# Kernel optimization log

Hardware: AMD Instinct MI355X
Metric: run time of the kernel (lower is better)

The kernel has to match this reference:

```python
import jax, jax.numpy as jnp
import numpy as np

B, C, H, W = 8, 256, 64, 64
CI = 128  # inter_channels = in_channels // reduction

def _conv1x1(x, w, b):
    # x: [b, c, h, w], w: [o, c], b: [o]
    return jnp.einsum('bchw,oc->bohw', x, w) + b[None, :, None, None]

def setup_inputs() -> dict:
    key = jax.random.key(0)
    ks = jax.random.split(key, 5)
    s_in = 1.0 / np.sqrt(C)
    s_ci = 1.0 / np.sqrt(CI)
    return {
        'x': jax.random.normal(ks[0], (B, C, H, W), jnp.float32),
        'w_g': jax.random.normal(ks[1], (CI, C), jnp.float32) * s_in,
        'b_g': jnp.zeros((CI,), jnp.float32),
        'w_theta': jax.random.normal(ks[2], (CI, C), jnp.float32) * s_in,
        'b_theta': jnp.zeros((CI,), jnp.float32),
        'w_phi': jax.random.normal(ks[3], (CI, C), jnp.float32) * s_in,
        'b_phi': jnp.zeros((CI,), jnp.float32),
        'w_out': jax.random.normal(ks[4], (C, CI), jnp.float32) * s_ci,
        'b_out': jnp.zeros((C,), jnp.float32),
    }

def reference(x, w_g, b_g, w_theta, b_theta, w_phi, b_phi, w_out, b_out):
    n, c, h, w = x.shape
    N = h * w
    g_x = _conv1x1(x, w_g, b_g).reshape(n, CI, N).transpose(0, 2, 1)        # [b, N, ci]
    theta_x = _conv1x1(x, w_theta, b_theta).reshape(n, CI, N).transpose(0, 2, 1)  # [b, N, ci]
    phi_x = _conv1x1(x, w_phi, b_phi).reshape(n, CI, N)                     # [b, ci, N]
    pw = jnp.einsum('bnc,bcm->bnm', theta_x, phi_x)                         # [b, N, N]
    # Faithful to source: divides by ci**(-0.5) == multiplies by sqrt(ci)
    pw = pw / (jnp.asarray(CI, x.dtype) ** -0.5)
    pw = jax.nn.softmax(pw, axis=-1)
    y = jnp.einsum('bnm,bmc->bnc', pw, g_x)                                 # [b, N, ci]
    y = y.transpose(0, 2, 1).reshape(n, CI, h, w)
    return x + _conv1x1(y, w_out, b_out)
```

## Files before the change

kernel.cpp:

```cpp
#include <hip/hip_runtime.h>
#include <hip/hip_bf16.h>
#include <stdint.h>
#include <stddef.h>


typedef __bf16 bf16;
typedef __attribute__((ext_vector_type(8))) __bf16 bf16x8;
typedef __attribute__((ext_vector_type(4))) __bf16 bf16x4;
typedef __attribute__((ext_vector_type(4))) float  f32x4;
typedef __attribute__((ext_vector_type(4))) int    i32x4;

#define MFMA16(a, b, c) __builtin_amdgcn_mfma_f32_16x16x32_bf16((a), (b), (c), 0, 0, 0)

constexpr int NB  = 8;
constexpr int NC  = 256;
constexpr int NN  = 4096;
constexpr int NCI = 128;
constexpr size_t NEL = (size_t)NB * NN * NCI;

__global__ __launch_bounds__(256) void k_proj(
    const float* __restrict__ x,
    const float* __restrict__ wt, const float* __restrict__ bt,
    const float* __restrict__ wp, const float* __restrict__ bp,
    const float* __restrict__ wg, const float* __restrict__ bg,
    bf16* __restrict__ qh, bf16* __restrict__ ql,
    bf16* __restrict__ kh, bf16* __restrict__ kl,
    bf16* __restrict__ vv)
{
    const int nt  = blockIdx.x;
    const int pj  = blockIdx.y;
    const int b   = blockIdx.z;
    const int tid = threadIdx.x;
    const int wv  = tid >> 6;
    const int ln  = tid & 63;
    const int lg  = ln >> 4;
    const int lq  = ln & 15;

    const float* W;
    const float* bias;
    if (pj == 0)      { W = wt; bias = bt; }
    else if (pj == 1) { W = wp; bias = bp; }
    else              { W = wg; bias = bg; }
    const bool split = (pj != 2);

    __shared__ char lds[49152];
    char* Ah = lds;
    char* Al = lds + 8192;
    char* Wh = lds + 16384;
    char* Wl = lds + 32768;

    f32x4 acc[8];
#pragma unroll
    for (int j = 0; j < 8; ++j) acc[j] = f32x4{0.f, 0.f, 0.f, 0.f};

    const int n0 = nt * 64;

    for (int c0 = 0; c0 < NC; c0 += 64) {
        __syncthreads();
#pragma unroll
        for (int p = 0; p < 4; ++p) {
            int cc = p * 16 + (tid >> 4);
            int nn = (tid & 15) * 4;
            f32x4 xv = *(const f32x4*)(x + ((size_t)b * NC + (c0 + cc)) * NN + n0 + nn);
#pragma unroll
            for (int e = 0; e < 4; ++e) {
                float f = xv[e];
                bf16 h = (bf16)f;
                int row = nn + e;
                int off = (row * 128 + cc * 2) ^ ((row & 7) << 4);
                *(bf16*)(Ah + off) = h;
                *(bf16*)(Al + off) = (bf16)(f - (float)h);
            }
        }
#pragma unroll
        for (int p = 0; p < 8; ++p) {
            int i  = p * 16 + (tid >> 4);
            int c4 = (tid & 15) * 4;
            f32x4 w4 = *(const f32x4*)(W + (size_t)i * NC + c0 + c4);
            bf16x4 hv, lv;
#pragma unroll
            for (int e = 0; e < 4; ++e) {
                bf16 h = (bf16)w4[e];
                hv[e] = h;
                lv[e] = (bf16)(w4[e] - (float)h);
            }
            int off = (i * 128 + c4 * 2) ^ ((i & 7) << 4);
            *(bf16x4*)(Wh + off) = hv;
            if (split) *(bf16x4*)(Wl + off) = lv;
        }
        __syncthreads();
#pragma unroll
        for (int kk = 0; kk < 2; ++kk) {
            int row  = wv * 16 + lq;
            int koff = kk * 64 + lg * 16;
            int aoff = (row * 128 + koff) ^ ((row & 7) << 4);
            bf16x8 ah = *(const bf16x8*)(Ah + aoff);
            bf16x8 al = *(const bf16x8*)(Al + aoff);
#pragma unroll
            for (int j = 0; j < 8; ++j) {
                int ir   = j * 16 + lq;
                int woff = (ir * 128 + koff) ^ ((ir & 7) << 4);
                bf16x8 bh = *(const bf16x8*)(Wh + woff);
                acc[j] = MFMA16(ah, bh, acc[j]);
                if (split) {
                    bf16x8 bl = *(const bf16x8*)(Wl + woff);
                    acc[j] = MFMA16(ah, bl, acc[j]);
                    acc[j] = MFMA16(al, bh, acc[j]);
                }
            }
        }
    }

    if (pj == 2) {
        __syncthreads();
        char* T = lds;
#pragma unroll
        for (int j = 0; j < 8; ++j) {
            int i = j * 16 + lq;
            float bv = bias[i];
#pragma unroll
            for (int r = 0; r < 4; ++r) {
                int nl = wv * 16 + lg * 4 + r;
                int off = (i * 128 + nl * 2) ^ ((i & 7) << 4);
                *(bf16*)(T + off) = (bf16)(acc[j][r] + bv);
            }
        }
        __syncthreads();
#pragma unroll
        for (int p = 0; p < 4; ++p) {
            int i  = p * 32 + (tid >> 3);
            int sl = tid & 7;
            i32x4 t = *(const i32x4*)(T + ((i * 128 + sl * 16) ^ ((i & 7) << 4)));
            *(i32x4*)(vv + ((size_t)b * NCI + i) * NN + n0 + sl * 8) = t;
        }
    } else {
#pragma unroll
        for (int j = 0; j < 8; ++j) {
            int i = j * 16 + lq;
            float bv = bias[i];
#pragma unroll
            for (int r = 0; r < 4; ++r) {
                int q = n0 + wv * 16 + lg * 4 + r;
                size_t off = ((size_t)b * NN + q) * NCI + i;
                float val = acc[j][r] + bv;
                bf16 h = (bf16)val;
                bf16 l = (bf16)(val - (float)h);
                if (pj == 0) { qh[off] = h; ql[off] = l; }
                else         { kh[off] = h; kl[off] = l; }
            }
        }
    }
}

__global__ __launch_bounds__(256, 2) void k_attn(
    const bf16* __restrict__ qh, const bf16* __restrict__ ql,
    const bf16* __restrict__ kh, const bf16* __restrict__ kl,
    const bf16* __restrict__ vt, bf16* __restrict__ y)
{
    const int bid = blockIdx.x;
    const int b   = bid & 7;
    const int qt  = bid >> 3;
    const int tid = threadIdx.x;
    const int wv  = tid >> 6;
    const int ln  = tid & 63;
    const int lg  = ln >> 4;
    const int lq  = ln & 15;
    const int n0  = qt * 64;

    __shared__ char lds[57344];
    char* KH = lds;
    char* KL = lds + 16384;
    char* VT = lds + 32768;
    char* P  = lds + 49152 + wv * 2048;

    bf16x8 qhf[4], qlf[4];
    {
        int qrow = n0 + wv * 16 + lq;
        const bf16* bh = qh + ((size_t)b * NN + qrow) * NCI;
        const bf16* bl = ql + ((size_t)b * NN + qrow) * NCI;
#pragma unroll
        for (int kk = 0; kk < 4; ++kk) {
            int d0 = kk * 32 + lg * 8;
            qhf[kk] = *(const bf16x8*)(bh + d0);
            qlf[kk] = *(const bf16x8*)(bl + d0);
        }
    }

    f32x4 o[8];
#pragma unroll
    for (int j = 0; j < 8; ++j) o[j] = f32x4{0.f, 0.f, 0.f, 0.f};
    float mrun = -1e30f, lrun = 0.f;
    const float scale = 11.313708498984761f;

    for (int m0 = 0; m0 < NN; m0 += 64) {
        __syncthreads();
#pragma unroll
        for (int p = 0; p < 4; ++p) {
            int mm = p * 16 + (tid >> 4);
            int sl = tid & 15;
            size_t g = ((size_t)b * NN + m0 + mm) * NCI + sl * 8;
            int off = (mm * 256 + sl * 16) ^ ((mm & 7) << 4);
            *(i32x4*)(KH + off) = *(const i32x4*)(kh + g);
            *(i32x4*)(KL + off) = *(const i32x4*)(kl + g);
        }
#pragma unroll
        for (int p = 0; p < 4; ++p) {
            int d  = p * 32 + (tid >> 3);
            int sl = tid & 7;
            size_t g = ((size_t)b * NCI + d) * NN + m0 + sl * 8;
            int off = (d * 128 + sl * 16) ^ ((d & 7) << 4);
            *(i32x4*)(VT + off) = *(const i32x4*)(vt + g);
        }
        __syncthreads();

        float pv[4][4];
        __builtin_amdgcn_s_setprio(1);
#pragma unroll
        for (int jm = 0; jm < 4; ++jm) {
            f32x4 s = f32x4{0.f, 0.f, 0.f, 0.f};
            int mrow = jm * 16 + lq;
#pragma unroll
            for (int kk = 0; kk < 4; ++kk) {
                int aoff = (mrow * 256 + kk * 64 + lg * 16) ^ ((mrow & 7) << 4);
                bf16x8 ah = *(const bf16x8*)(KH + aoff);
                bf16x8 al = *(const bf16x8*)(KL + aoff);
                s = MFMA16(ah, qhf[kk], s);
                s = MFMA16(al, qhf[kk], s);
                s = MFMA16(ah, qlf[kk], s);
            }
#pragma unroll
            for (int r = 0; r < 4; ++r) pv[jm][r] = s[r] * scale;
        }
        __builtin_amdgcn_s_setprio(0);

        float tmax = pv[0][0];
#pragma unroll
        for (int jm = 0; jm < 4; ++jm)
#pragma unroll
            for (int r = 0; r < 4; ++r) tmax = fmaxf(tmax, pv[jm][r]);
        tmax = fmaxf(tmax, __shfl_xor(tmax, 16));
        tmax = fmaxf(tmax, __shfl_xor(tmax, 32));
        float mnew = fmaxf(mrun, tmax);
        float alpha = __expf(mrun - mnew);
        mrun = mnew;
        float psum = 0.f;
#pragma unroll
        for (int jm = 0; jm < 4; ++jm)
#pragma unroll
            for (int r = 0; r < 4; ++r) {
                pv[jm][r] = __expf(pv[jm][r] - mnew);
                psum += pv[jm][r];
            }
        psum += __shfl_xor(psum, 16);
        psum += __shfl_xor(psum, 32);
        lrun = lrun * alpha + psum;

#pragma unroll
        for (int jm = 0; jm < 4; ++jm) {
            bf16x4 pk;
#pragma unroll
            for (int r = 0; r < 4; ++r) pk[r] = (bf16)pv[jm][r];
            int off = (lq * 128 + (jm * 16 + lg * 4) * 2) ^ ((lq & 7) << 4);
            *(bf16x4*)(P + off) = pk;
        }

        float av[4];
#pragma unroll
        for (int r = 0; r < 4; ++r) av[r] = __shfl(alpha, lg * 4 + r);
#pragma unroll
        for (int j = 0; j < 8; ++j)
#pragma unroll
            for (int r = 0; r < 4; ++r) o[j][r] *= av[r];

        bf16x8 pa[2];
#pragma unroll
        for (int t = 0; t < 2; ++t)
            pa[t] = *(const bf16x8*)(P + ((lq * 128 + t * 64 + lg * 16) ^ ((lq & 7) << 4)));
        __builtin_amdgcn_s_setprio(1);
#pragma unroll
        for (int j = 0; j < 8; ++j) {
            int d = j * 16 + lq;
#pragma unroll
            for (int t = 0; t < 2; ++t) {
                bf16x8 bv = *(const bf16x8*)(VT + ((d * 128 + t * 64 + lg * 16) ^ ((d & 7) << 4)));
                o[j] = MFMA16(pa[t], bv, o[j]);
            }
        }
        __builtin_amdgcn_s_setprio(0);
    }

    float lr[4];
#pragma unroll
    for (int r = 0; r < 4; ++r) lr[r] = __shfl(lrun, lg * 4 + r);
#pragma unroll
    for (int j = 0; j < 8; ++j) {
        int d = j * 16 + lq;
#pragma unroll
        for (int r = 0; r < 4; ++r) {
            int q = n0 + wv * 16 + lg * 4 + r;
            y[((size_t)b * NN + q) * NCI + d] = (bf16)(o[j][r] / lr[r]);
        }
    }
}

__global__ __launch_bounds__(256) void k_out(
    const bf16* __restrict__ y, const float* __restrict__ x,
    const float* __restrict__ w_out, const float* __restrict__ b_out,
    float* __restrict__ out)
{
    const int nt  = blockIdx.x;
    const int b   = blockIdx.y;
    const int tid = threadIdx.x;
    const int wv  = tid >> 6;
    const int ln  = tid & 63;
    const int lg  = ln >> 4;
    const int lq  = ln & 15;
    const int n0  = nt * 64;

    __shared__ char Y[16384];
#pragma unroll
    for (int p = 0; p < 4; ++p) {
        int nn = p * 16 + (tid >> 4);
        int d0 = (tid & 15) * 8;
        i32x4 t = *(const i32x4*)(y + ((size_t)b * NN + n0 + nn) * NCI + d0);
        *(i32x4*)(Y + ((nn * 256 + d0 * 2) ^ ((nn & 7) << 4))) = t;
    }
    __syncthreads();

    bf16x8 af[4];
    {
        int row = wv * 16 + lq;
#pragma unroll
        for (int kk = 0; kk < 4; ++kk) {
            int koff = kk * 64 + lg * 16;
            af[kk] = *(const bf16x8*)(Y + ((row * 256 + koff) ^ ((row & 7) << 4)));
        }
    }

    f32x4 acc[16];
#pragma unroll
    for (int j = 0; j < 16; ++j) acc[j] = f32x4{0.f, 0.f, 0.f, 0.f};

#pragma unroll
    for (int j = 0; j < 16; ++j) {
        int c = j * 16 + lq;
#pragma unroll
        for (int kk = 0; kk < 4; ++kk) {
            int i0 = kk * 32 + lg * 8;
            f32x4 wa = *(const f32x4*)(w_out + (size_t)c * NCI + i0);
            f32x4 wb = *(const f32x4*)(w_out + (size_t)c * NCI + i0 + 4);
            bf16x8 bw;
#pragma unroll
            for (int e = 0; e < 4; ++e) { bw[e] = (bf16)wa[e]; bw[e + 4] = (bf16)wb[e]; }
            acc[j] = MFMA16(af[kk], bw, acc[j]);
        }
    }

#pragma unroll
    for (int j = 0; j < 16; ++j) {
        int c = j * 16 + lq;
        int nb = n0 + wv * 16 + lg * 4;
        size_t off = ((size_t)b * NC + c) * (size_t)NN + nb;
        f32x4 xv = *(const f32x4*)(x + off);
        float bo = b_out[c];
        f32x4 r;
#pragma unroll
        for (int t = 0; t < 4; ++t) r[t] = acc[j][t] + xv[t] + bo;
        *(f32x4*)(out + off) = r;
    }
}

extern "C" void kernel_launch(void* const* d_in, const int* in_sizes, int n_in,
                              void* d_out, int out_size, void* d_ws, size_t ws_size,
                              hipStream_t stream)
{
    (void)in_sizes; (void)n_in; (void)out_size; (void)ws_size;
    const float* x  = (const float*)d_in[0];
    const float* wg = (const float*)d_in[1];
    const float* bg = (const float*)d_in[2];
    const float* wt = (const float*)d_in[3];
    const float* bt = (const float*)d_in[4];
    const float* wp = (const float*)d_in[5];
    const float* bp = (const float*)d_in[6];
    const float* wo = (const float*)d_in[7];
    const float* bo = (const float*)d_in[8];
    float* out = (float*)d_out;

    char* ws = (char*)d_ws;
    bf16* qh = (bf16*)(ws);
    bf16* ql = (bf16*)(ws + NEL * 2);
    bf16* kh = (bf16*)(ws + NEL * 4);
    bf16* kl = (bf16*)(ws + NEL * 6);
    bf16* vv = (bf16*)(ws + NEL * 8);
    bf16* y  = qh;

    k_proj<<<dim3(64, 3, 8), 256, 0, stream>>>(x, wt, bt, wp, bp, wg, bg,
                                               qh, ql, kh, kl, vv);
    k_attn<<<dim3(512), 256, 0, stream>>>(qh, ql, kh, kl, vv, y);
    k_out<<<dim3(64, 8), 256, 0, stream>>>(y, x, wo, bo, out);
}
```

Baseline: 255.4 us.

## Double-buffer K/V tiles and process two query tiles per wave in attention

The attention kernel now handles 128 query rows per block, with each wave covering 32 rows, so every K/V fragment read from LDS feeds two MFMA chains. K/V tiles are double-buffered in LDS and the next tile's global loads are issued through registers while the current tile computes, which cuts the loop to one barrier per tile. Together these aim to halve LDS and global traffic per query and hide load latency. In exchange the grid drops to 256 blocks, occupancy falls to one block per CU under larger LDS and register use, and there are fewer waves to hide latency.

Measured after the change: 278.6 us. 1.09x slower.

```diff
diff --git a/kernel.cpp b/kernel.cpp
--- a/kernel.cpp
+++ b/kernel.cpp
@@ -152,7 +152,7 @@
     }
 }
 
-__global__ __launch_bounds__(256, 2) void k_attn(
+__global__ __launch_bounds__(256, 1) void k_attn(
     const bf16* __restrict__ qh, const bf16* __restrict__ ql,
     const bf16* __restrict__ kh, const bf16* __restrict__ kl,
     const bf16* __restrict__ vt, bf16* __restrict__ y)
@@ -165,140 +165,226 @@
     const int ln  = tid & 63;
     const int lg  = ln >> 4;
     const int lq  = ln & 15;
-    const int n0  = qt * 64;
-
-    __shared__ char lds[57344];
-    char* KH = lds;
-    char* KL = lds + 16384;
-    char* VT = lds + 32768;
-    char* P  = lds + 49152 + wv * 2048;
-
-    bf16x8 qhf[4], qlf[4];
-    {
-        int qrow = n0 + wv * 16 + lq;
+    const int n0  = qt * 128;
+
+    __shared__ __attribute__((aligned(16))) char lds[114688];
+    char* P = lds + 98304 + wv * 4096;
+
+    const int smm = tid >> 4;
+    const int ssl = tid & 15;
+    const int svd = tid >> 3;
+    const int svl = tid & 7;
+
+    bf16x8 qhf[2][4], qlf[2][4];
+#pragma unroll
+    for (int q2 = 0; q2 < 2; ++q2) {
+        int qrow = n0 + wv * 32 + q2 * 16 + lq;
         const bf16* bh = qh + ((size_t)b * NN + qrow) * NCI;
         const bf16* bl = ql + ((size_t)b * NN + qrow) * NCI;
 #pragma unroll
         for (int kk = 0; kk < 4; ++kk) {
-            int d0 = kk * 32 + lg * 8;
-            qhf[kk] = *(const bf16x8*)(bh + d0);
-            qlf[kk] = *(const bf16x8*)(bl + d0);
-        }
-    }
-
-    f32x4 o[8];
-#pragma unroll
-    for (int j = 0; j < 8; ++j) o[j] = f32x4{0.f, 0.f, 0.f, 0.f};
-    float mrun = -1e30f, lrun = 0.f;
+            qhf[q2][kk] = *(const bf16x8*)(bh + kk * 32 + lg * 8);
+            qlf[q2][kk] = *(const bf16x8*)(bl + kk * 32 + lg * 8);
+        }
+    }
+
+    f32x4 o[2][8];
+#pragma unroll
+    for (int q2 = 0; q2 < 2; ++q2)
+#pragma unroll
+        for (int j = 0; j < 8; ++j) o[q2][j] = f32x4{0.f, 0.f, 0.f, 0.f};
+    float mrun[2] = {-1e30f, -1e30f};
+    float lrun[2] = {0.f, 0.f};
     const float scale = 11.313708498984761f;
 
-    for (int m0 = 0; m0 < NN; m0 += 64) {
-        __syncthreads();
+    {
 #pragma unroll
         for (int p = 0; p < 4; ++p) {
-            int mm = p * 16 + (tid >> 4);
-            int sl = tid & 15;
-            size_t g = ((size_t)b * NN + m0 + mm) * NCI + sl * 8;
-            int off = (mm * 256 + sl * 16) ^ ((mm & 7) << 4);
-            *(i32x4*)(KH + off) = *(const i32x4*)(kh + g);
-            *(i32x4*)(KL + off) = *(const i32x4*)(kl + g);
+            int mm = p * 16 + smm;
+            size_t g = ((size_t)b * NN + mm) * NCI + ssl * 8;
+            i32x4 h = *(const i32x4*)(kh + g);
+            i32x4 l = *(const i32x4*)(kl + g);
+            int off = (mm * 256 + ssl * 16) ^ ((mm & 7) << 4);
+            *(i32x4*)(lds + off) = h;
+            *(i32x4*)(lds + 16384 + off) = l;
         }
 #pragma unroll
         for (int p = 0; p < 4; ++p) {
-            int d  = p * 32 + (tid >> 3);
-            int sl = tid & 7;
-            size_t g = ((size_t)b * NCI + d) * NN + m0 + sl * 8;
-            int off = (d * 128 + sl * 16) ^ ((d & 7) << 4);
-            *(i32x4*)(VT + off) = *(const i32x4*)(vt + g);
-        }
-        __syncthreads();
-
-        float pv[4][4];
+            int d = p * 32 + svd;
+            size_t g = ((size_t)b * NCI + d) * NN + svl * 8;
+            i32x4 v = *(const i32x4*)(vt + g);
+            int off = (d * 128 + svl * 16) ^ ((d & 7) << 4);
+            *(i32x4*)(lds + 32768 + off) = v;
+        }
+    }
+    __syncthreads();
+
+    for (int t = 0; t < 64; ++t) {
+        const int cur = t & 1;
+        char* KH  = lds + cur * 49152;
+        char* KL  = KH + 16384;
+        char* VT  = KH + 32768;
+        char* KHn = lds + (cur ^ 1) * 49152;
+        char* KLn = KHn + 16384;
+        char* VTn = KHn + 32768;
+        const int m0n = (t + 1) * 64;
+        const bool pre = (t < 63);
+
+        i32x4 rkh[4], rkl[4];
+        if (pre) {
+#pragma unroll
+            for (int p = 0; p < 4; ++p) {
+                size_t g = ((size_t)b * NN + m0n + p * 16 + smm) * NCI + ssl * 8;
+                rkh[p] = *(const i32x4*)(kh + g);
+                rkl[p] = *(const i32x4*)(kl + g);
+            }
+        }
+
+        f32x4 s[4][2];
         __builtin_amdgcn_s_setprio(1);
 #pragma unroll
         for (int jm = 0; jm < 4; ++jm) {
-            f32x4 s = f32x4{0.f, 0.f, 0.f, 0.f};
-            int mrow = jm * 16 + lq;
+            s[jm][0] = f32x4{0.f, 0.f, 0.f, 0.f};
+            s[jm][1] = f32x4{0.f, 0.f, 0.f, 0.f};
+            const int mrow = jm * 16 + lq;
+            const int sw = (mrow & 7) << 4;
 #pragma unroll
             for (int kk = 0; kk < 4; ++kk) {
-                int aoff = (mrow * 256 + kk * 64 + lg * 16) ^ ((mrow & 7) << 4);
+                int aoff = (mrow * 256 + kk * 64 + lg * 16) ^ sw;
                 bf16x8 ah = *(const bf16x8*)(KH + aoff);
                 bf16x8 al = *(const bf16x8*)(KL + aoff);
-                s = MFMA16(ah, qhf[kk], s);
-                s = MFMA16(al, qhf[kk], s);
-                s = MFMA16(ah, qlf[kk], s);
-            }
-#pragma unroll
-            for (int r = 0; r < 4; ++r) pv[jm][r] = s[r] * scale;
+                s[jm][0] = MFMA16(ah, qhf[0][kk], s[jm][0]);
+                s[jm][1] = MFMA16(ah, qhf[1][kk], s[jm][1]);
+                s[jm][0] = MFMA16(al, qhf[0][kk], s[jm][0]);
+                s[jm][1] = MFMA16(al, qhf[1][kk], s[jm][1]);
+                s[jm][0] = MFMA16(ah, qlf[0][kk], s[jm][0]);
+                s[jm][1] = MFMA16(ah, qlf[1][kk], s[jm][1]);
+            }
         }
         __builtin_amdgcn_s_setprio(0);
 
-        float tmax = pv[0][0];
+        i32x4 rv[4];
+        if (pre) {
+#pragma unroll
+            for (int p = 0; p < 4; ++p) {
+                int mm = p * 16 + smm;
+                int off = (mm * 256 + ssl * 16) ^ ((mm & 7) << 4);
+                *(i32x4*)(KHn + off) = rkh[p];
+                *(i32x4*)(KLn + off) = rkl[p];
+            }
+#pragma unroll
+            for (int p = 0; p < 4; ++p) {
+                size_t g = ((size_t)b * NCI + p * 32 + svd) * NN + m0n + svl * 8;
+                rv[p] = *(const i32x4*)(vt + g);
+            }
+        }
+
+        float tm[2];
+        tm[0] = s[0][0][0];
+        tm[1] = s[0][1][0];
 #pragma unroll
         for (int jm = 0; jm < 4; ++jm)
 #pragma unroll
-            for (int r = 0; r < 4; ++r) tmax = fmaxf(tmax, pv[jm][r]);
-        tmax = fmaxf(tmax, __shfl_xor(tmax, 16));
-        tmax = fmaxf(tmax, __shfl_xor(tmax, 32));
-        float mnew = fmaxf(mrun, tmax);
-        float alpha = __expf(mrun - mnew);
-        mrun = mnew;
-        float psum = 0.f;
+            for (int r = 0; r < 4; ++r) {
+                tm[0] = fmaxf(tm[0], s[jm][0][r]);
+                tm[1] = fmaxf(tm[1], s[jm][1][r]);
+            }
+#pragma unroll
+        for (int q2 = 0; q2 < 2; ++q2) {
+            tm[q2] = fmaxf(tm[q2], __shfl_xor(tm[q2], 16));
+            tm[q2] = fmaxf(tm[q2], __shfl_xor(tm[q2], 32));
+        }
+        float alpha[2], psum[2];
+#pragma unroll
+        for (int q2 = 0; q2 < 2; ++q2) {
+            float mnew = fmaxf(mrun[q2], tm[q2] * scale);
+            alpha[q2] = __expf(mrun[q2] - mnew);
+            mrun[q2] = mnew;
+            psum[q2] = 0.f;
+        }
 #pragma unroll
         for (int jm = 0; jm < 4; ++jm)
 #pragma unroll
+            for (int q2 = 0; q2 < 2; ++q2) {
+                bf16x4 pk;
+#pragma unroll
+                for (int r = 0; r < 4; ++r) {
+                    float e = __expf(s[jm][q2][r] * scale - mrun[q2]);
+                    psum[q2] += e;
+                    pk[r] = (bf16)e;
+                }
+                int row = q2 * 16 + lq;
+                int off = (row * 128 + (jm * 16 + lg * 4) * 2) ^ ((lq & 7) << 4);
+                *(bf16x4*)(P + off) = pk;
+            }
+#pragma unroll
+        for (int q2 = 0; q2 < 2; ++q2) {
+            psum[q2] += __shfl_xor(psum[q2], 16);
+            psum[q2] += __shfl_xor(psum[q2], 32);
+            lrun[q2] = lrun[q2] * alpha[q2] + psum[q2];
+        }
+
+        float av0[4], av1[4];
+#pragma unroll
+        for (int r = 0; r < 4; ++r) {
+            av0[r] = __shfl(alpha[0], lg * 4 + r);
+            av1[r] = __shfl(alpha[1], lg * 4 + r);
+        }
+#pragma unroll
+        for (int j = 0; j < 8; ++j)
+#pragma unroll
             for (int r = 0; r < 4; ++r) {
-                pv[jm][r] = __expf(pv[jm][r] - mnew);
-                psum += pv[jm][r];
-            }
-        psum += __shfl_xor(psum, 16);
-        psum += __shfl_xor(psum, 32);
-        lrun = lrun * alpha + psum;
-
-#pragma unroll
-        for (int jm = 0; jm < 4; ++jm) {
-            bf16x4 pk;
-#pragma unroll
-            for (int r = 0; r < 4; ++r) pk[r] = (bf16)pv[jm][r];
-            int off = (lq * 128 + (jm * 16 + lg * 4) * 2) ^ ((lq & 7) << 4);
-            *(bf16x4*)(P + off) = pk;
-        }
-
-        float av[4];
-#pragma unroll
-        for (int r = 0; r < 4; ++r) av[r] = __shfl(alpha, lg * 4 + r);
-#pragma unroll
-        for (int j = 0; j < 8; ++j)
-#pragma unroll
-            for (int r = 0; r < 4; ++r) o[j][r] *= av[r];
-
-        bf16x8 pa[2];
-#pragma unroll
-        for (int t = 0; t < 2; ++t)
-            pa[t] = *(const bf16x8*)(P + ((lq * 128 + t * 64 + lg * 16) ^ ((lq & 7) << 4)));
+                o[0][j][r] *= av0[r];
+                o[1][j][r] *= av1[r];
+            }
+
+        bf16x8 pa[2][2];
+#pragma unroll
+        for (int q2 = 0; q2 < 2; ++q2)
+#pragma unroll
+            for (int tt = 0; tt < 2; ++tt) {
+                int row = q2 * 16 + lq;
+                pa[q2][tt] = *(const bf16x8*)(P + ((row * 128 + tt * 64 + lg * 16) ^ ((lq & 7) << 4)));
+            }
         __builtin_amdgcn_s_setprio(1);
 #pragma unroll
         for (int j = 0; j < 8; ++j) {
             int d = j * 16 + lq;
-#pragma unroll
-            for (int t = 0; t < 2; ++t) {
-                bf16x8 bv = *(const bf16x8*)(VT + ((d * 128 + t * 64 + lg * 16) ^ ((d & 7) << 4)));
-                o[j] = MFMA16(pa[t], bv, o[j]);
+            int swv = (lq & 7) << 4;
+#pragma unroll
+            for (int tt = 0; tt < 2; ++tt) {
+                bf16x8 bv = *(const bf16x8*)(VT + ((d * 128 + tt * 64 + lg * 16) ^ swv));
+                o[0][j] = MFMA16(pa[0][tt], bv, o[0][j]);
+                o[1][j] = MFMA16(pa[1][tt], bv, o[1][j]);
             }
         }
         __builtin_amdgcn_s_setprio(0);
-    }
-
-    float lr[4];
-#pragma unroll
-    for (int r = 0; r < 4; ++r) lr[r] = __shfl(lrun, lg * 4 + r);
+
+        if (pre) {
+#pragma unroll
+            for (int p = 0; p < 4; ++p) {
+                int d = p * 32 + svd;
+                int off = (d * 128 + svl * 16) ^ ((d & 7) << 4);
+                *(i32x4*)(VTn + off) = rv[p];
+            }
+        }
+        __syncthreads();
+    }
+
+    float rl0[4], rl1[4];
+#pragma unroll
+    for (int r = 0; r < 4; ++r) {
+        rl0[r] = 1.f / __shfl(lrun[0], lg * 4 + r);
+        rl1[r] = 1.f / __shfl(lrun[1], lg * 4 + r);
+    }
 #pragma unroll
     for (int j = 0; j < 8; ++j) {
         int d = j * 16 + lq;
 #pragma unroll
         for (int r = 0; r < 4; ++r) {
-            int q = n0 + wv * 16 + lg * 4 + r;
-            y[((size_t)b * NN + q) * NCI + d] = (bf16)(o[j][r] / lr[r]);
+            int q0 = n0 + wv * 32 + lg * 4 + r;
+            y[((size_t)b * NN + q0) * NCI + d]      = (bf16)(o[0][j][r] * rl0[r]);
+            y[((size_t)b * NN + q0 + 16) * NCI + d] = (bf16)(o[1][j][r] * rl1[r]);
         }
     }
 }
@@ -396,6 +482,6 @@
 
     k_proj<<<dim3(64, 3, 8), 256, 0, stream>>>(x, wt, bt, wp, bp, wg, bg,
                                                qh, ql, kh, kl, vv);
-    k_attn<<<dim3(512), 256, 0, stream>>>(qh, ql, kh, kl, vv, y);
+    k_attn<<<dim3(256), 256, 0, stream>>>(qh, ql, kh, kl, vv, y);
     k_out<<<dim3(64, 8), 256, 0, stream>>>(y, x, wo, bo, out);
 }
```

## Pre-swizzle V into MFMA fragment layout, fold scale into Q, lazy softmax rescale

Applied to the files above, without the earlier changes.

The projection kernel now writes V in a layout already arranged as MFMA B-fragments, so the attention kernel loads V straight from global memory into registers instead of staging it through LDS. This shrinks LDS use and removes one shared-memory pass per tile. The softmax scale and log2(e) are folded into Q at projection time, and the kernel uses exp2f with a conditional rescale that only runs when the row max grows by more than a threshold. The trade-off is higher register pressure from holding 16 V fragments, and the lazy rescale lets exponents exceed 1 by up to 2^8 before bf16 rounding.

Result: slower. 264.5 us (+3.6%).

```diff
diff --git a/kernel.cpp b/kernel.cpp
--- a/kernel.cpp
+++ b/kernel.cpp
@@ -17,6 +17,10 @@
 constexpr int NN  = 4096;
 constexpr int NCI = 128;
 constexpr size_t NEL = (size_t)NB * NN * NCI;
+constexpr int PBATCH = NN * NCI;
+
+#define QSCALE (11.313708498984761f * 1.4426950408889634f)
+
 
 __global__ __launch_bounds__(256) void k_proj(
     const float* __restrict__ x,
@@ -65,11 +69,11 @@
 #pragma unroll
             for (int e = 0; e < 4; ++e) {
                 float f = xv[e];
-                bf16 h = (bf16)f;
+                bf16 hh = (bf16)f;
                 int row = nn + e;
                 int off = (row * 128 + cc * 2) ^ ((row & 7) << 4);
-                *(bf16*)(Ah + off) = h;
-                *(bf16*)(Al + off) = (bf16)(f - (float)h);
+                *(bf16*)(Ah + off) = hh;
+                *(bf16*)(Al + off) = (bf16)(f - (float)hh);
             }
         }
 #pragma unroll
@@ -80,9 +84,9 @@
             bf16x4 hv, lv;
 #pragma unroll
             for (int e = 0; e < 4; ++e) {
-                bf16 h = (bf16)w4[e];
-                hv[e] = h;
-                lv[e] = (bf16)(w4[e] - (float)h);
+                bf16 hh = (bf16)w4[e];
+                hv[e] = hh;
+                lv[e] = (bf16)(w4[e] - (float)hh);
             }
             int off = (i * 128 + c4 * 2) ^ ((i & 7) << 4);
             *(bf16x4*)(Wh + off) = hv;
@@ -117,12 +121,12 @@
 #pragma unroll
         for (int j = 0; j < 8; ++j) {
             int i = j * 16 + lq;
-            float bv = bias[i];
+            float bv2 = bias[i];
 #pragma unroll
             for (int r = 0; r < 4; ++r) {
                 int nl = wv * 16 + lg * 4 + r;
                 int off = (i * 128 + nl * 2) ^ ((i & 7) << 4);
-                *(bf16*)(T + off) = (bf16)(acc[j][r] + bv);
+                *(bf16*)(T + off) = (bf16)(acc[j][r] + bv2);
             }
         }
         __syncthreads();
@@ -130,23 +134,27 @@
         for (int p = 0; p < 4; ++p) {
             int i  = p * 32 + (tid >> 3);
             int sl = tid & 7;
-            i32x4 t = *(const i32x4*)(T + ((i * 128 + sl * 16) ^ ((i & 7) << 4)));
-            *(i32x4*)(vv + ((size_t)b * NCI + i) * NN + n0 + sl * 8) = t;
+            i32x4 tv = *(const i32x4*)(T + ((i * 128 + sl * 16) ^ ((i & 7) << 4)));
+            size_t off = (size_t)b * PBATCH
+                       + (size_t)((((nt * 8 + (i >> 4)) * 2 + (sl >> 2)) * 64
+                                   + (sl & 3) * 16 + (i & 15)) * 8);
+            *(i32x4*)(vv + off) = tv;
         }
     } else {
+        const float sc = (pj == 0) ? QSCALE : 1.0f;
 #pragma unroll
         for (int j = 0; j < 8; ++j) {
             int i = j * 16 + lq;
-            float bv = bias[i];
+            float bv2 = bias[i];
 #pragma unroll
             for (int r = 0; r < 4; ++r) {
                 int q = n0 + wv * 16 + lg * 4 + r;
                 size_t off = ((size_t)b * NN + q) * NCI + i;
-                float val = acc[j][r] + bv;
-                bf16 h = (bf16)val;
-                bf16 l = (bf16)(val - (float)h);
-                if (pj == 0) { qh[off] = h; ql[off] = l; }
-                else         { kh[off] = h; kl[off] = l; }
+                float val = (acc[j][r] + bv2) * sc;
+                bf16 hh = (bf16)val;
+                bf16 ll = (bf16)(val - (float)hh);
+                if (pj == 0) { qh[off] = hh; ql[off] = ll; }
+                else         { kh[off] = hh; kl[off] = ll; }
             }
         }
     }
@@ -155,7 +163,7 @@
 __global__ __launch_bounds__(256, 2) void k_attn(
     const bf16* __restrict__ qh, const bf16* __restrict__ ql,
     const bf16* __restrict__ kh, const bf16* __restrict__ kl,
-    const bf16* __restrict__ vt, bf16* __restrict__ y)
+    const bf16* __restrict__ vf, bf16* __restrict__ y)
 {
     const int bid = blockIdx.x;
     const int b   = bid & 7;
@@ -167,11 +175,10 @@
     const int lq  = ln & 15;
     const int n0  = qt * 64;
 
-    __shared__ char lds[57344];
+    __shared__ __attribute__((aligned(16))) char lds[40960];
     char* KH = lds;
     char* KL = lds + 16384;
-    char* VT = lds + 32768;
-    char* P  = lds + 49152 + wv * 2048;
+    char* P  = lds + 32768 + wv * 2048;
 
     bf16x8 qhf[4], qlf[4];
     {
@@ -190,7 +197,8 @@
 #pragma unroll
     for (int j = 0; j < 8; ++j) o[j] = f32x4{0.f, 0.f, 0.f, 0.f};
     float mrun = -1e30f, lrun = 0.f;
-    const float scale = 11.313708498984761f;
+
+    const bf16* vb = vf + (size_t)b * PBATCH + (size_t)ln * 8;
 
     for (int m0 = 0; m0 < NN; m0 += 64) {
         __syncthreads();
@@ -203,102 +211,99 @@
             *(i32x4*)(KH + off) = *(const i32x4*)(kh + g);
             *(i32x4*)(KL + off) = *(const i32x4*)(kl + g);
         }
-#pragma unroll
-        for (int p = 0; p < 4; ++p) {
-            int d  = p * 32 + (tid >> 3);
-            int sl = tid & 7;
-            size_t g = ((size_t)b * NCI + d) * NN + m0 + sl * 8;
-            int off = (d * 128 + sl * 16) ^ ((d & 7) << 4);
-            *(i32x4*)(VT + off) = *(const i32x4*)(vt + g);
-        }
-        __syncthreads();
-
-        float pv[4][4];
+        __syncthreads();
+
+        bf16x8 bv[8][2];
+        {
+            const bf16* vp = vb + (size_t)(m0 >> 6) * 8192;
+#pragma unroll
+            for (int j = 0; j < 8; ++j) {
+                bv[j][0] = *(const bf16x8*)(vp + (j * 2 + 0) * 512);
+                bv[j][1] = *(const bf16x8*)(vp + (j * 2 + 1) * 512);
+            }
+        }
+
+        f32x4 s[4];
         __builtin_amdgcn_s_setprio(1);
 #pragma unroll
         for (int jm = 0; jm < 4; ++jm) {
-            f32x4 s = f32x4{0.f, 0.f, 0.f, 0.f};
-            int mrow = jm * 16 + lq;
+            s[jm] = f32x4{0.f, 0.f, 0.f, 0.f};
+            const int mrow = jm * 16 + lq;
+            const int sw = (mrow & 7) << 4;
 #pragma unroll
             for (int kk = 0; kk < 4; ++kk) {
-                int aoff = (mrow * 256 + kk * 64 + lg * 16) ^ ((mrow & 7) << 4);
+                int aoff = (mrow * 256 + kk * 64 + lg * 16) ^ sw;
                 bf16x8 ah = *(const bf16x8*)(KH + aoff);
                 bf16x8 al = *(const bf16x8*)(KL + aoff);
-                s = MFMA16(ah, qhf[kk], s);
-                s = MFMA16(al, qhf[kk], s);
-                s = MFMA16(ah, qlf[kk], s);
-            }
-#pragma unroll
-            for (int r = 0; r < 4; ++r) pv[jm][r] = s[r] * scale;
+                s[jm] = MFMA16(ah, qhf[kk], s[jm]);
+                s[jm] = MFMA16(al, qhf[kk], s[jm]);
+                s[jm] = MFMA16(ah, qlf[kk], s[jm]);
+            }
         }
         __builtin_amdgcn_s_setprio(0);
 
-        float tmax = pv[0][0];
+        float tm = s[0][0];
 #pragma unroll
         for (int jm = 0; jm < 4; ++jm)
 #pragma unroll
-            for (int r = 0; r < 4; ++r) tmax = fmaxf(tmax, pv[jm][r]);
-        tmax = fmaxf(tmax, __shfl_xor(tmax, 16));
-        tmax = fmaxf(tmax, __shfl_xor(tmax, 32));
-        float mnew = fmaxf(mrun, tmax);
-        float alpha = __expf(mrun - mnew);
-        mrun = mnew;
+            for (int r = 0; r < 4; ++r) tm = fmaxf(tm, s[jm][r]);
+        tm = fmaxf(tm, __shfl_xor(tm, 16));
+        tm = fmaxf(tm, __shfl_xor(tm, 32));
+
+        if (__any(tm > mrun + 8.f)) {
+            float mnew = fmaxf(mrun, tm);
+            float alpha = exp2f(mrun - mnew);
+            mrun = mnew;
+            lrun *= alpha;
+            float av[4];
+#pragma unroll
+            for (int r = 0; r < 4; ++r) av[r] = __shfl(alpha, lg * 4 + r);
+#pragma unroll
+            for (int j = 0; j < 8; ++j)
+#pragma unroll
+                for (int r = 0; r < 4; ++r) o[j][r] *= av[r];
+        }
+
         float psum = 0.f;
 #pragma unroll
-        for (int jm = 0; jm < 4; ++jm)
+        for (int jm = 0; jm < 4; ++jm) {
+            bf16x4 pk;
 #pragma unroll
             for (int r = 0; r < 4; ++r) {
-                pv[jm][r] = __expf(pv[jm][r] - mnew);
-                psum += pv[jm][r];
-            }
+                float e2 = exp2f(s[jm][r] - mrun);
+                psum += e2;
+                pk[r] = (bf16)e2;
+            }
+            int off = (lq * 128 + (jm * 16 + lg * 4) * 2) ^ ((lq & 7) << 4);
+            *(bf16x4*)(P + off) = pk;
+        }
         psum += __shfl_xor(psum, 16);
         psum += __shfl_xor(psum, 32);
-        lrun = lrun * alpha + psum;
-
-#pragma unroll
-        for (int jm = 0; jm < 4; ++jm) {
-            bf16x4 pk;
-#pragma unroll
-            for (int r = 0; r < 4; ++r) pk[r] = (bf16)pv[jm][r];
-            int off = (lq * 128 + (jm * 16 + lg * 4) * 2) ^ ((lq & 7) << 4);
-            *(bf16x4*)(P + off) = pk;
-        }
-
-        float av[4];
-#pragma unroll
-        for (int r = 0; r < 4; ++r) av[r] = __shfl(alpha, lg * 4 + r);
-#pragma unroll
-        for (int j = 0; j < 8; ++j)
-#pragma unroll
-            for (int r = 0; r < 4; ++r) o[j][r] *= av[r];
+        lrun += psum;
 
         bf16x8 pa[2];
 #pragma unroll
-        for (int t = 0; t < 2; ++t)
-            pa[t] = *(const bf16x8*)(P + ((lq * 128 + t * 64 + lg * 16) ^ ((lq & 7) << 4)));
+        for (int tt = 0; tt < 2; ++tt)
+            pa[tt] = *(const bf16x8*)(P + ((lq * 128 + tt * 64 + lg * 16) ^ ((lq & 7) << 4)));
         __builtin_amdgcn_s_setprio(1);
 #pragma unroll
         for (int j = 0; j < 8; ++j) {
-            int d = j * 16 + lq;
-#pragma unroll
-            for (int t = 0; t < 2; ++t) {
-                bf16x8 bv = *(const bf16x8*)(VT + ((d * 128 + t * 64 + lg * 16) ^ ((d & 7) << 4)));
-                o[j] = MFMA16(pa[t], bv, o[j]);
-            }
+            o[j] = MFMA16(pa[0], bv[j][0], o[j]);
+            o[j] = MFMA16(pa[1], bv[j][1], o[j]);
         }
         __builtin_amdgcn_s_setprio(0);
     }
 
-    float lr[4];
-#pragma unroll
-    for (int r = 0; r < 4; ++r) lr[r] = __shfl(lrun, lg * 4 + r);
+    float rl[4];
+#pragma unroll
+    for (int r = 0; r < 4; ++r) rl[r] = 1.f / __shfl(lrun, lg * 4 + r);
 #pragma unroll
     for (int j = 0; j < 8; ++j) {
         int d = j * 16 + lq;
 #pragma unroll
         for (int r = 0; r < 4; ++r) {
             int q = n0 + wv * 16 + lg * 4 + r;
-            y[((size_t)b * NN + q) * NCI + d] = (bf16)(o[j][r] / lr[r]);
+            y[((size_t)b * NN + q) * NCI + d] = (bf16)(o[j][r] * rl[r]);
         }
     }
 }
```
